# Optimization experiments

Measured on AMD Instinct MI355X. Metric: run time of the kernel, lower is better.

The kernel has to match this reference:

```python
import jax, jax.numpy as jnp
import numpy as np

D_MODEL = 128


def setup_inputs() -> dict:
    key = jax.random.key(0)
    ks = jax.random.split(key, 7)
    d = D_MODEL
    B, N = 4, 512
    # Kaiming-ish init scales for linear layers
    W1 = jax.random.normal(ks[0], (2 * d, d), jnp.float32) / np.sqrt(2 * d)
    b1 = jnp.zeros((d,), jnp.float32)
    W2 = jax.random.normal(ks[1], (d, d // 2), jnp.float32) / np.sqrt(d)
    b2 = jnp.zeros((d // 2,), jnp.float32)
    W3 = jax.random.normal(ks[2], (d // 2, 1), jnp.float32) / np.sqrt(d // 2)
    b3 = jnp.zeros((1,), jnp.float32)
    node_features = jax.random.normal(ks[3], (B, N, d), jnp.float32)
    return {"node_features": node_features, "W1": W1, "b1": b1,
            "W2": W2, "b2": b2, "W3": W3, "b3": b3}


def reference(node_features, W1, b1, W2, b2, W3, b3):
    # node_features: [B, N, d]. Pairwise concat [x_i, x_j] @ W1 is split as
    # x_i @ W1[:d] + x_j @ W1[d:] — same math as cat+Linear, but avoids
    # materializing the [B, N, N, 2d] concat tensor.
    d = node_features.shape[-1]
    hi = jnp.einsum('bnd,dk->bnk', node_features, W1[:d])   # [B, N, d]
    hj = jnp.einsum('bnd,dk->bnk', node_features, W1[d:])   # [B, N, d]
    h = jax.nn.relu(hi[:, :, None, :] + hj[:, None, :, :] + b1)  # [B, N, N, d]
    h = jax.nn.relu(jnp.einsum('bijk,km->bijm', h, W2) + b2)      # [B, N, N, d/2]
    logits = jnp.einsum('bijm,mo->bijo', h, W3) + b3              # [B, N, N, 1]
    return jax.nn.sigmoid(logits[..., 0])                          # [B, N, N]
```

## Files before the change

### kernel.cpp

```cpp
#include <hip/hip_runtime.h>
#include <hip/hip_fp16.h>

#define D_MODEL 128
#define NB 4
#define NN 512

typedef _Float16 f16;
typedef _Float16 f16x8 __attribute__((ext_vector_type(8)));
typedef float f32x4 __attribute__((ext_vector_type(4)));

__global__ __launch_bounds__(256) void prep_kernel(
    const float* __restrict__ x,
    const float* __restrict__ W1,
    const float* __restrict__ b1,
    const float* __restrict__ W2,
    f16* __restrict__ Hi, f16* __restrict__ Hj, f16* __restrict__ W2p)
{
    const int blk = blockIdx.x;
    const int t = threadIdx.x;
    if (blk < 256) {
        const int r0 = blk * 8;
        __shared__ float xs[8][128];
        for (int idx = t; idx < 8 * 128; idx += 256)
            xs[idx >> 7][idx & 127] = x[(size_t)r0 * 128 + idx];
        __syncthreads();

        const int isJ = t >> 7;
        const int k = t & 127;
        const float* wcol = W1 + (isJ ? 128 * 128 : 0) + k;
        float acc[8];
        #pragma unroll
        for (int r = 0; r < 8; r++) acc[r] = 0.f;
        for (int d = 0; d < 128; d++) {
            float w = wcol[d * 128];
            #pragma unroll
            for (int r = 0; r < 8; r++) acc[r] = fmaf(xs[r][d], w, acc[r]);
        }
        const float bb = isJ ? 0.f : b1[k];
        f16* dst = isJ ? Hj : Hi;
        #pragma unroll
        for (int r = 0; r < 8; r++)
            dst[(size_t)(r0 + r) * 128 + k] = (f16)(acc[r] + bb);
    } else {
        for (int slot = t; slot < 16 * 64; slot += 256) {
            const int lane = slot & 63;
            const int fidx = slot >> 6;
            const int kt = fidx >> 2, nt = fidx & 3;
            const int krow = kt * 32 + 8 * (lane >> 4);
            const int col = nt * 16 + (lane & 15);
            #pragma unroll
            for (int j = 0; j < 8; j++)
                W2p[(size_t)slot * 8 + j] = (f16)W2[(krow + j) * 64 + col];
        }
    }
}

__global__ __launch_bounds__(256, 4) void pair_kernel(
    const f16* __restrict__ Hi, const f16* __restrict__ Hj,
    const f16* __restrict__ W2p,
    const float* __restrict__ b2, const float* __restrict__ W3,
    const float* __restrict__ b3p, float* __restrict__ out)
{
    const int lane = threadIdx.x & 63;
    const int wave = threadIdx.x >> 6;
    const int bid = blockIdx.x;
    const int jg4 = bid & 7;
    const int ic  = (bid >> 3) & 31;
    const int b   = bid >> 8;
    const int j0 = (jg4 * 4 + wave) * 16;
    const int i0 = ic * 16;

    const int lrow = lane & 15;
    const int lgrp = lane >> 4;

    f16x8 w2f[4][4];
    #pragma unroll
    for (int kt = 0; kt < 4; kt++)
        #pragma unroll
        for (int nt = 0; nt < 4; nt++)
            w2f[kt][nt] = *(const f16x8*)(W2p + (size_t)((kt * 4 + nt) * 64 + lane) * 8);

    const f16* hjbase = Hj + (size_t)(b * NN + j0 + lrow) * 128 + 8 * lgrp;
    f16x8 hjf[4];
    #pragma unroll
    for (int kt = 0; kt < 4; kt++)
        hjf[kt] = *(const f16x8*)(hjbase + kt * 32);

    f32x4 b2v[4], w3v[4];
    #pragma unroll
    for (int nt = 0; nt < 4; nt++) {
        b2v[nt] = *(const f32x4*)(b2 + nt * 16 + 4 * lgrp);
        w3v[nt] = *(const f32x4*)(W3 + nt * 16 + 4 * lgrp);
    }
    const float b3 = b3p[0];

    const f16* hibase = Hi + (size_t)(b * NN + i0) * 128 + 8 * lgrp;
    float* orow = out + ((size_t)b * NN + i0) * NN + j0 + lrow;

    const f16x8 zero8 = (f16x8)(f16)0;

    #pragma unroll 2
    for (int ii = 0; ii < 16; ii++) {
        f16x8 hif[4];
        #pragma unroll
        for (int kt = 0; kt < 4; kt++)
            hif[kt] = *(const f16x8*)(hibase + ii * 128 + kt * 32);

        f32x4 accD[4];
        #pragma unroll
        for (int nt = 0; nt < 4; nt++) accD[nt] = (f32x4)(0.0f);

        #pragma unroll
        for (int kt = 0; kt < 4; kt++) {
            f16x8 s = hif[kt] + hjf[kt];
            s = __builtin_elementwise_max(s, zero8);
            #pragma unroll
            for (int nt = 0; nt < 4; nt++)
                accD[nt] = __builtin_amdgcn_mfma_f32_16x16x32_f16(w2f[kt][nt], s, accD[nt], 0, 0, 0);
        }

        float acc = 0.f;
        #pragma unroll
        for (int nt = 0; nt < 4; nt++) {
            #pragma unroll
            for (int r = 0; r < 4; r++) {
                float h = fmaxf(accD[nt][r] + b2v[nt][r], 0.f);
                acc = fmaf(h, w3v[nt][r], acc);
            }
        }
        acc += __shfl_xor(acc, 16, 64);
        acc += __shfl_xor(acc, 32, 64);
        float sg = __builtin_amdgcn_rcpf(1.f + __expf(-(acc + b3)));
        if (lgrp == 0)
            orow[(size_t)ii * NN] = sg;
    }
}

extern "C" void kernel_launch(void* const* d_in, const int* in_sizes, int n_in,
                              void* d_out, int out_size, void* d_ws, size_t ws_size,
                              hipStream_t stream) {
    const float* x  = (const float*)d_in[0];
    const float* W1 = (const float*)d_in[1];
    const float* b1 = (const float*)d_in[2];
    const float* W2 = (const float*)d_in[3];
    const float* b2 = (const float*)d_in[4];
    const float* W3 = (const float*)d_in[5];
    const float* b3 = (const float*)d_in[6];
    float* out = (float*)d_out;

    f16* Hi  = (f16*)d_ws;
    f16* Hj  = Hi + (size_t)NB * NN * 128;
    f16* W2p = Hj + (size_t)NB * NN * 128;

    prep_kernel<<<257, 256, 0, stream>>>(x, W1, b1, W2, Hi, Hj, W2p);
    pair_kernel<<<1024, 256, 0, stream>>>(Hi, Hj, W2p, b2, W3, b3, out);
}
```

Baseline: 123.0 us.

## Halve per-block work, remap block order, vectorize prep loads, nontemporal output stores

The prep kernel now handles 4 rows per block over 513 blocks and reads shared x as float4 vectors. The pair kernel launches 2048 blocks of 8 i-rows each, with a permuted block index that interleaves the j-groups across the launch order. Empty asm barriers keep W2 and Hj fragments pinned in registers, and the sigmoid outputs are written with nontemporal stores. The aim is better load balance and occupancy across CUs plus less cache pollution from output writes. The cost is reloading W2/Hj fragments twice as often per output row.

Measured after the change: 127.0 us. 3.3% more time.

```diff
diff --git a/kernel.cpp b/kernel.cpp
--- a/kernel.cpp
+++ b/kernel.cpp
@@ -18,28 +18,34 @@
 {
     const int blk = blockIdx.x;
     const int t = threadIdx.x;
-    if (blk < 256) {
-        const int r0 = blk * 8;
-        __shared__ float xs[8][128];
-        for (int idx = t; idx < 8 * 128; idx += 256)
+    if (blk < 512) {
+        const int r0 = blk * 4;
+        __shared__ float xs[4][128];
+        #pragma unroll
+        for (int idx = t; idx < 4 * 128; idx += 256)
             xs[idx >> 7][idx & 127] = x[(size_t)r0 * 128 + idx];
         __syncthreads();
 
         const int isJ = t >> 7;
         const int k = t & 127;
         const float* wcol = W1 + (isJ ? 128 * 128 : 0) + k;
-        float acc[8];
-        #pragma unroll
-        for (int r = 0; r < 8; r++) acc[r] = 0.f;
-        for (int d = 0; d < 128; d++) {
-            float w = wcol[d * 128];
+        float acc[4] = {0.f, 0.f, 0.f, 0.f};
+        #pragma unroll 4
+        for (int d4 = 0; d4 < 32; d4++) {
+            f32x4 xv[4];
             #pragma unroll
-            for (int r = 0; r < 8; r++) acc[r] = fmaf(xs[r][d], w, acc[r]);
+            for (int r = 0; r < 4; r++) xv[r] = *(const f32x4*)&xs[r][d4 * 4];
+            #pragma unroll
+            for (int dd = 0; dd < 4; dd++) {
+                float w = wcol[(d4 * 4 + dd) * 128];
+                #pragma unroll
+                for (int r = 0; r < 4; r++) acc[r] = fmaf(xv[r][dd], w, acc[r]);
+            }
         }
         const float bb = isJ ? 0.f : b1[k];
         f16* dst = isJ ? Hj : Hi;
         #pragma unroll
-        for (int r = 0; r < 8; r++)
+        for (int r = 0; r < 4; r++)
             dst[(size_t)(r0 + r) * 128 + k] = (f16)(acc[r] + bb);
     } else {
         for (int slot = t; slot < 16 * 64; slot += 256) {
@@ -63,12 +69,13 @@
 {
     const int lane = threadIdx.x & 63;
     const int wave = threadIdx.x >> 6;
-    const int bid = blockIdx.x;
-    const int jg4 = bid & 7;
-    const int ic  = (bid >> 3) & 31;
-    const int b   = bid >> 8;
+
+    const int logical = (blockIdx.x & 7) * 256 + (blockIdx.x >> 3);
+    const int jg4 = logical & 7;
+    const int ic  = (logical >> 3) & 63;
+    const int b   = logical >> 9;
     const int j0 = (jg4 * 4 + wave) * 16;
-    const int i0 = ic * 16;
+    const int i0 = ic * 8;
 
     const int lrow = lane & 15;
     const int lgrp = lane >> 4;
@@ -77,14 +84,18 @@
     #pragma unroll
     for (int kt = 0; kt < 4; kt++)
         #pragma unroll
-        for (int nt = 0; nt < 4; nt++)
+        for (int nt = 0; nt < 4; nt++) {
             w2f[kt][nt] = *(const f16x8*)(W2p + (size_t)((kt * 4 + nt) * 64 + lane) * 8);
+            asm volatile("" : "+v"(w2f[kt][nt]));
+        }
 
     const f16* hjbase = Hj + (size_t)(b * NN + j0 + lrow) * 128 + 8 * lgrp;
     f16x8 hjf[4];
     #pragma unroll
-    for (int kt = 0; kt < 4; kt++)
+    for (int kt = 0; kt < 4; kt++) {
         hjf[kt] = *(const f16x8*)(hjbase + kt * 32);
+        asm volatile("" : "+v"(hjf[kt]));
+    }
 
     f32x4 b2v[4], w3v[4];
     #pragma unroll
@@ -100,7 +111,7 @@
     const f16x8 zero8 = (f16x8)(f16)0;
 
     #pragma unroll 2
-    for (int ii = 0; ii < 16; ii++) {
+    for (int ii = 0; ii < 8; ii++) {
         f16x8 hif[4];
         #pragma unroll
         for (int kt = 0; kt < 4; kt++)
@@ -132,7 +143,7 @@
         acc += __shfl_xor(acc, 32, 64);
         float sg = __builtin_amdgcn_rcpf(1.f + __expf(-(acc + b3)));
         if (lgrp == 0)
-            orow[(size_t)ii * NN] = sg;
+            __builtin_nontemporal_store(sg, orow + (size_t)ii * NN);
     }
 }
 
@@ -152,6 +163,6 @@
     f16* Hj  = Hi + (size_t)NB * NN * 128;
     f16* W2p = Hj + (size_t)NB * NN * 128;
 
-    prep_kernel<<<257, 256, 0, stream>>>(x, W1, b1, W2, Hi, Hj, W2p);
-    pair_kernel<<<1024, 256, 0, stream>>>(Hi, Hj, W2p, b2, W3, b3, out);
+    prep_kernel<<<513, 256, 0, stream>>>(x, W1, b1, W2, Hi, Hj, W2p);
+    pair_kernel<<<2048, 256, 0, stream>>>(Hi, Hj, W2p, b2, W3, b3, out);
 }
```
